# Kernel optimization log

Measured on AMD Instinct MI355X. Metric: run time of the kernel, lower is better.

## Reference

```python
import jax, jax.numpy as jnp
import numpy as np


def setup_inputs() -> dict:
    key = jax.random.key(0)
    ks = jax.random.split(key, 8)
    C, R = 256, 16
    Cqk = C // R  # 16
    B, H, W = 8, 64, 64
    x = jax.random.normal(ks[0], (B, C, H, W), dtype=jnp.float32)
    # 1x1 conv weights stored as [out, in] (kernel dims squeezed)
    s = 1.0 / np.sqrt(C)
    Wq = jax.random.uniform(ks[1], (Cqk, C), minval=-s, maxval=s, dtype=jnp.float32)
    bq = jax.random.uniform(ks[2], (Cqk,), minval=-s, maxval=s, dtype=jnp.float32)
    Wk = jax.random.uniform(ks[3], (Cqk, C), minval=-s, maxval=s, dtype=jnp.float32)
    bk = jax.random.uniform(ks[4], (Cqk,), minval=-s, maxval=s, dtype=jnp.float32)
    Wv = jax.random.uniform(ks[5], (C, C), minval=-s, maxval=s, dtype=jnp.float32)
    bv = jax.random.uniform(ks[6], (C,), minval=-s, maxval=s, dtype=jnp.float32)
    gamma = jnp.float32(0.1)  # nonzero so the attention branch affects output
    return {"x": x, "Wq": Wq, "bq": bq, "Wk": Wk, "bk": bk, "Wv": Wv, "bv": bv, "gamma": gamma}


def reference(x, Wq, bq, Wk, bk, Wv, bv, gamma):
    B, C, H, W = x.shape
    N = H * W
    xf = x.reshape(B, C, N)  # [B, C, N]
    # 1x1 convs == per-pixel linear over channel dim
    q = jnp.einsum('oc,bcn->bon', Wq, xf) + bq[None, :, None]  # [B, Cqk, N]
    k = jnp.einsum('oc,bcn->bon', Wk, xf) + bk[None, :, None]  # [B, Cqk, N]
    v = jnp.einsum('oc,bcn->bon', Wv, xf) + bv[None, :, None]  # [B, C, N]
    # scores[b, i, j] = q[:, i] . k[:, j]; no scale factor (faithful to source)
    scores = jnp.einsum('bdn,bdm->bnm', q, k)  # [B, N, N]
    attn = jax.nn.softmax(scores, axis=-1)
    # y[b, c, i] = sum_j v[b, c, j] * attn[b, i, j]
    y = jnp.einsum('bcm,bnm->bcn', v, attn).reshape(B, C, H, W)
    return x + gamma * y
```

## Files before the change

### kernel.cpp

```cpp
#include <hip/hip_runtime.h>
#include <hip/hip_bf16.h>
#include <math.h>

typedef short bf16x8 __attribute__((ext_vector_type(8)));
typedef float f32x4 __attribute__((ext_vector_type(4)));

#define MFMA_B16(A, B, C) __builtin_amdgcn_mfma_f32_16x16x32_bf16(A, B, C, 0, 0, 0)

#define NBATCH 8
#define CIN 256
#define NPIX 4096

__device__ __forceinline__ unsigned short f2b(float f) {
    union { float f; unsigned int u; } v;
    v.f = f;
    return (unsigned short)((v.u + 0x7fffu + ((v.u >> 16) & 1u)) >> 16);
}

__global__ __launch_bounds__(256, 2) void qkv_kernel(
    const float* __restrict__ x,
    const float* __restrict__ Wq, const float* __restrict__ bq,
    const float* __restrict__ Wk, const float* __restrict__ bk,
    const float* __restrict__ Wv, const float* __restrict__ bv,
    unsigned short* __restrict__ qT, unsigned short* __restrict__ kT,
    unsigned short* __restrict__ vv)
{
    constexpr int XSTR = 264;
    __shared__ __align__(16) unsigned short xs[64 * XSTR];
    const int b     = blockIdx.x >> 6;
    const int nbase = (blockIdx.x & 63) * 64;
    const int tid = threadIdx.x;
    const int w  = tid >> 6;
    const int l  = tid & 63;
    const int g  = l >> 4;
    const int ln = l & 15;

    {
        const float* xp = x + (size_t)b * CIN * NPIX + nbase + l;
        unsigned short* xsp = xs + l * XSTR + w * 64;
        #pragma unroll
        for (int cc = 0; cc < 32; ++cc) {
            float v0 = xp[(size_t)(w * 64 + 2 * cc)     * NPIX];
            float v1 = xp[(size_t)(w * 64 + 2 * cc + 1) * NPIX];
            unsigned int pk = (unsigned int)f2b(v0) | ((unsigned int)f2b(v1) << 16);
            *(unsigned int*)(xsp + 2 * cc) = pk;
        }
    }
    __syncthreads();

    const f32x4 vzero = {0.f, 0.f, 0.f, 0.f};
    f32x4 acc[4][4];
    f32x4 accq[4];
    #pragma unroll
    for (int i = 0; i < 4; ++i) {
        accq[i] = vzero;
        #pragma unroll
        for (int j = 0; j < 4; ++j) acc[i][j] = vzero;
    }

    for (int ks = 0; ks < 8; ++ks) {
        const int k0 = ks * 32;
        bf16x8 xf[4];
        #pragma unroll
        for (int nt = 0; nt < 4; ++nt)
            xf[nt] = *(const bf16x8*)(xs + (nt * 16 + ln) * XSTR + k0 + g * 8);
        #pragma unroll
        for (int ct = 0; ct < 4; ++ct) {
            const float* wp = Wv + (size_t)(w * 64 + ct * 16 + ln) * CIN + k0 + g * 8;
            bf16x8 wf;
            #pragma unroll
            for (int j = 0; j < 8; ++j) wf[j] = (short)f2b(wp[j]);
            #pragma unroll
            for (int nt = 0; nt < 4; ++nt)
                acc[ct][nt] = MFMA_B16(wf, xf[nt], acc[ct][nt]);
        }
        if (w < 2) {
            const float* wqk = (w == 0 ? Wq : Wk) + (size_t)ln * CIN + k0 + g * 8;
            bf16x8 wf;
            #pragma unroll
            for (int j = 0; j < 8; ++j) wf[j] = (short)f2b(wqk[j]);
            #pragma unroll
            for (int nt = 0; nt < 4; ++nt)
                accq[nt] = MFMA_B16(wf, xf[nt], accq[nt]);
        }
    }

    #pragma unroll
    for (int ct = 0; ct < 4; ++ct) {
        #pragma unroll
        for (int r = 0; r < 4; ++r) {
            const int c = w * 64 + ct * 16 + g * 4 + r;
            const float bias = bv[c];
            #pragma unroll
            for (int nt = 0; nt < 4; ++nt)
                vv[((size_t)b * CIN + c) * NPIX + nbase + nt * 16 + ln] =
                    f2b(acc[ct][nt][r] + bias);
        }
    }
    if (w < 2) {
        unsigned short* oq = (w == 0 ? qT : kT);
        const float* bias  = (w == 0 ? bq : bk);
        #pragma unroll
        for (int r = 0; r < 4; ++r) {
            const int d = g * 4 + r;
            const float bi = bias[d];
            #pragma unroll
            for (int nt = 0; nt < 4; ++nt)
                oq[((size_t)b * NPIX + nbase + nt * 16 + ln) * 32 + d] =
                    f2b(accq[nt][r] + bi);
        }
    } else {
        unsigned short* oq = (w == 2 ? qT : kT);
        unsigned short* p  = oq + ((size_t)b * NPIX + nbase + l) * 32 + 16;
        uint4 z; z.x = 0; z.y = 0; z.z = 0; z.w = 0;
        *(uint4*)p       = z;
        *(uint4*)(p + 8) = z;
    }
}

__global__ __launch_bounds__(256, 2) void attn_kernel(
    const float* __restrict__ x, const float* __restrict__ gamma_p,
    const unsigned short* __restrict__ qT, const unsigned short* __restrict__ kT,
    const unsigned short* __restrict__ vv, float* __restrict__ out)
{
    constexpr int PSTR = 72;
    __shared__ __align__(16) unsigned short P_lds[64 * PSTR];
    __shared__ __align__(16) float smax[64 * 4];
    __shared__ __align__(16) float ssum[64 * 4];
    const int b     = blockIdx.x & 7;
    const int qbase = (blockIdx.x >> 3) * 64;
    const int tid = threadIdx.x;
    const int w  = tid >> 6;
    const int l  = tid & 63;
    const int g  = l >> 4;
    const int ln = l & 15;
    const float gamma = *gamma_p;

    bf16x8 qf[4];
    #pragma unroll
    for (int qt = 0; qt < 4; ++qt)
        qf[qt] = *(const bf16x8*)(qT + ((size_t)b * NPIX + qbase + qt * 16 + ln) * 32 + g * 8);

    const f32x4 vzero = {0.f, 0.f, 0.f, 0.f};
    f32x4 acc[4][4];
    #pragma unroll
    for (int i = 0; i < 4; ++i) {
        #pragma unroll
        for (int j = 0; j < 4; ++j) acc[i][j] = vzero;
    }
    float m_run[4] = {-INFINITY, -INFINITY, -INFINITY, -INFINITY};
    float l_run[4] = {0.f, 0.f, 0.f, 0.f};

    for (int kt = 0; kt < 64; ++kt) {
        const int k0 = kt * 64;
        const bf16x8 kf = *(const bf16x8*)(kT + ((size_t)b * NPIX + k0 + w * 16 + ln) * 32 + g * 8);
        f32x4 s[4];
        #pragma unroll
        for (int qt = 0; qt < 4; ++qt)
            s[qt] = MFMA_B16(kf, qf[qt], vzero);

        float pm[4];
        #pragma unroll
        for (int qt = 0; qt < 4; ++qt) {
            float m = fmaxf(fmaxf(s[qt][0], s[qt][1]), fmaxf(s[qt][2], s[qt][3]));
            m = fmaxf(m, __shfl_xor(m, 16));
            m = fmaxf(m, __shfl_xor(m, 32));
            pm[qt] = m;
        }
        if (g == 0) {
            #pragma unroll
            for (int qt = 0; qt < 4; ++qt) smax[(qt * 16 + ln) * 4 + w] = pm[qt];
        }
        __syncthreads();

        float m_new[4], scale[4], ps[4];
        #pragma unroll
        for (int qt = 0; qt < 4; ++qt) {
            f32x4 t = *(const f32x4*)(smax + (qt * 16 + ln) * 4);
            float tm = fmaxf(fmaxf(t[0], t[1]), fmaxf(t[2], t[3]));
            m_new[qt] = fmaxf(m_run[qt], tm);
            scale[qt] = __expf(m_run[qt] - m_new[qt]);
        }
        #pragma unroll
        for (int qt = 0; qt < 4; ++qt) {
            float p0 = __expf(s[qt][0] - m_new[qt]);
            float p1 = __expf(s[qt][1] - m_new[qt]);
            float p2 = __expf(s[qt][2] - m_new[qt]);
            float p3 = __expf(s[qt][3] - m_new[qt]);
            float sum = (p0 + p1) + (p2 + p3);
            sum += __shfl_xor(sum, 16);
            sum += __shfl_xor(sum, 32);
            ps[qt] = sum;
            uint2 pk;
            pk.x = (unsigned int)f2b(p0) | ((unsigned int)f2b(p1) << 16);
            pk.y = (unsigned int)f2b(p2) | ((unsigned int)f2b(p3) << 16);
            *(uint2*)(P_lds + (qt * 16 + ln) * PSTR + w * 16 + g * 4) = pk;
        }
        if (g == 0) {
            #pragma unroll
            for (int qt = 0; qt < 4; ++qt) ssum[(qt * 16 + ln) * 4 + w] = ps[qt];
        }
        __syncthreads();

        #pragma unroll
        for (int qt = 0; qt < 4; ++qt) {
            f32x4 t = *(const f32x4*)(ssum + (qt * 16 + ln) * 4);
            l_run[qt] = l_run[qt] * scale[qt] + ((t[0] + t[1]) + (t[2] + t[3]));
            m_run[qt] = m_new[qt];
            #pragma unroll
            for (int ct = 0; ct < 4; ++ct) {
                acc[qt][ct][0] *= scale[qt];
                acc[qt][ct][1] *= scale[qt];
                acc[qt][ct][2] *= scale[qt];
                acc[qt][ct][3] *= scale[qt];
            }
        }

        #pragma unroll
        for (int kk = 0; kk < 2; ++kk) {
            bf16x8 pf[4];
            #pragma unroll
            for (int qt = 0; qt < 4; ++qt)
                pf[qt] = *(const bf16x8*)(P_lds + (qt * 16 + ln) * PSTR + kk * 32 + g * 8);
            #pragma unroll
            for (int ct = 0; ct < 4; ++ct) {
                const bf16x8 vf = *(const bf16x8*)(
                    vv + ((size_t)b * CIN + w * 64 + ct * 16 + ln) * NPIX + k0 + kk * 32 + g * 8);
                #pragma unroll
                for (int qt = 0; qt < 4; ++qt)
                    acc[qt][ct] = MFMA_B16(vf, pf[qt], acc[qt][ct]);
            }
        }
    }

    #pragma unroll
    for (int qt = 0; qt < 4; ++qt) {
        const float inv = 1.0f / l_run[qt];
        const int n = qbase + qt * 16 + ln;
        #pragma unroll
        for (int ct = 0; ct < 4; ++ct) {
            #pragma unroll
            for (int r = 0; r < 4; ++r) {
                const int c = w * 64 + ct * 16 + g * 4 + r;
                const size_t idx = ((size_t)b * CIN + c) * NPIX + n;
                out[idx] = x[idx] + gamma * (acc[qt][ct][r] * inv);
            }
        }
    }
}

extern "C" void kernel_launch(void* const* d_in, const int* in_sizes, int n_in,
                              void* d_out, int out_size, void* d_ws, size_t ws_size,
                              hipStream_t stream) {
    const float* x     = (const float*)d_in[0];
    const float* Wq    = (const float*)d_in[1];
    const float* bq    = (const float*)d_in[2];
    const float* Wk    = (const float*)d_in[3];
    const float* bk    = (const float*)d_in[4];
    const float* Wv    = (const float*)d_in[5];
    const float* bv    = (const float*)d_in[6];
    const float* gamma = (const float*)d_in[7];

    unsigned short* qT = (unsigned short*)d_ws;
    unsigned short* kT = qT + (size_t)NBATCH * NPIX * 32;
    unsigned short* vv = kT + (size_t)NBATCH * NPIX * 32;

    qkv_kernel<<<512, 256, 0, stream>>>(x, Wq, bq, Wk, bk, Wv, bv, qT, kT, vv);
    attn_kernel<<<512, 256, 0, stream>>>(x, gamma, qT, kT, vv, (float*)d_out);
}
```

Before: 331.7 us.

## Restructure attention to barrier-free per-wave softmax with lazy rescaling and prepacked weights

The attention kernel is reorganized so each wave owns 32 query rows across all 64 keys, with a 2x2 split over query and channel halves. This removes the shared-memory max/sum exchange and both block barriers; P is rearranged into the MFMA operand layout with cross-lane shuffles instead of going through LDS. Softmax switches to exp2 with log2(e) folded into Wq and bq, uses a hardware bf16 pack instruction, and only rescales the accumulators when the running max grows by more than a threshold. A new pre-kernel converts the weights to bf16 once so qkv_kernel loads packed weights instead of converting them per tile. The trade-offs are an extra launch, duplicated K loads and QK MFMAs across the waves that share a query half, and more shuffle traffic.

```diff
diff --git a/kernel.cpp b/kernel.cpp
--- a/kernel.cpp
+++ b/kernel.cpp
@@ -10,6 +10,8 @@
 #define NBATCH 8
 #define CIN 256
 #define NPIX 4096
+#define L2E 1.4426950408889634f
+#define THR2 8.0f
 
 __device__ __forceinline__ unsigned short f2b(float f) {
     union { float f; unsigned int u; } v;
@@ -17,11 +19,31 @@
     return (unsigned short)((v.u + 0x7fffu + ((v.u >> 16) & 1u)) >> 16);
 }
 
+__device__ __forceinline__ unsigned int cvtpk(float lo, float hi) {
+    unsigned int r;
+    asm volatile("v_cvt_pk_bf16_f32 %0, %1, %2" : "=v"(r) : "v"(lo), "v"(hi));
+    return r;
+}
+
+__global__ void packw_kernel(const float* __restrict__ Wq, const float* __restrict__ Wk,
+                             const float* __restrict__ Wv,
+                             unsigned short* __restrict__ wv_bf,
+                             unsigned short* __restrict__ wqk_bf) {
+    int t = blockIdx.x * 256 + threadIdx.x;
+    if (t < 65536) {
+        wv_bf[t] = f2b(Wv[t]);
+    } else {
+        int u = t - 65536;
+        int r = u >> 8, c = u & 255;
+        float v = (r < 16) ? Wq[r * 256 + c] * L2E : Wk[(r - 16) * 256 + c];
+        wqk_bf[u] = f2b(v);
+    }
+}
+
 __global__ __launch_bounds__(256, 2) void qkv_kernel(
     const float* __restrict__ x,
-    const float* __restrict__ Wq, const float* __restrict__ bq,
-    const float* __restrict__ Wk, const float* __restrict__ bk,
-    const float* __restrict__ Wv, const float* __restrict__ bv,
+    const unsigned short* __restrict__ wv_bf, const unsigned short* __restrict__ wqk_bf,
+    const float* __restrict__ bq, const float* __restrict__ bk, const float* __restrict__ bv,
     unsigned short* __restrict__ qT, unsigned short* __restrict__ kT,
     unsigned short* __restrict__ vv)
 {
@@ -66,22 +88,16 @@
             xf[nt] = *(const bf16x8*)(xs + (nt * 16 + ln) * XSTR + k0 + g * 8);
         #pragma unroll
         for (int ct = 0; ct < 4; ++ct) {
-            const float* wp = Wv + (size_t)(w * 64 + ct * 16 + ln) * CIN + k0 + g * 8;
-            bf16x8 wf;
-            #pragma unroll
-            for (int j = 0; j < 8; ++j) wf[j] = (short)f2b(wp[j]);
+            const bf16x8 wf = *(const bf16x8*)(wv_bf + (size_t)(w * 64 + ct * 16 + ln) * CIN + k0 + g * 8);
             #pragma unroll
             for (int nt = 0; nt < 4; ++nt)
                 acc[ct][nt] = MFMA_B16(wf, xf[nt], acc[ct][nt]);
         }
         if (w < 2) {
-            const float* wqk = (w == 0 ? Wq : Wk) + (size_t)ln * CIN + k0 + g * 8;
-            bf16x8 wf;
-            #pragma unroll
-            for (int j = 0; j < 8; ++j) wf[j] = (short)f2b(wqk[j]);
-            #pragma unroll
-            for (int nt = 0; nt < 4; ++nt)
-                accq[nt] = MFMA_B16(wf, xf[nt], accq[nt]);
+            const bf16x8 wfq = *(const bf16x8*)(wqk_bf + (size_t)(w * 16 + ln) * CIN + k0 + g * 8);
+            #pragma unroll
+            for (int nt = 0; nt < 4; ++nt)
+                accq[nt] = MFMA_B16(wfq, xf[nt], accq[nt]);
         }
     }
 
@@ -99,11 +115,10 @@
     }
     if (w < 2) {
         unsigned short* oq = (w == 0 ? qT : kT);
-        const float* bias  = (w == 0 ? bq : bk);
         #pragma unroll
         for (int r = 0; r < 4; ++r) {
             const int d = g * 4 + r;
-            const float bi = bias[d];
+            const float bi = (w == 0 ? bq[d] * L2E : bk[d]);
             #pragma unroll
             for (int nt = 0; nt < 4; ++nt)
                 oq[((size_t)b * NPIX + nbase + nt * 16 + ln) * 32 + d] =
@@ -123,125 +138,131 @@
     const unsigned short* __restrict__ qT, const unsigned short* __restrict__ kT,
     const unsigned short* __restrict__ vv, float* __restrict__ out)
 {
-    constexpr int PSTR = 72;
-    __shared__ __align__(16) unsigned short P_lds[64 * PSTR];
-    __shared__ __align__(16) float smax[64 * 4];
-    __shared__ __align__(16) float ssum[64 * 4];
     const int b     = blockIdx.x & 7;
     const int qbase = (blockIdx.x >> 3) * 64;
     const int tid = threadIdx.x;
-    const int w  = tid >> 6;
-    const int l  = tid & 63;
-    const int g  = l >> 4;
-    const int ln = l & 15;
+    const int wid = tid >> 6;
+    const int wq  = wid & 1;
+    const int wc  = wid >> 1;
+    const int l   = tid & 63;
+    const int ln  = l & 15;
+    const int g   = l >> 4;
     const float gamma = *gamma_p;
 
-    bf16x8 qf[4];
-    #pragma unroll
-    for (int qt = 0; qt < 4; ++qt)
-        qf[qt] = *(const bf16x8*)(qT + ((size_t)b * NPIX + qbase + qt * 16 + ln) * 32 + g * 8);
+    const int srcA = ln + ((g & 1) << 5);
+    const int srcB = srcA + 16;
+    const bool hi  = (g >> 1) != 0;
+
+    bf16x8 qf[2];
+    #pragma unroll
+    for (int qt = 0; qt < 2; ++qt)
+        qf[qt] = *(const bf16x8*)(qT + ((size_t)b * NPIX + qbase + wq * 32 + qt * 16 + ln) * 32 + g * 8);
 
     const f32x4 vzero = {0.f, 0.f, 0.f, 0.f};
-    f32x4 acc[4][4];
-    #pragma unroll
-    for (int i = 0; i < 4; ++i) {
-        #pragma unroll
-        for (int j = 0; j < 4; ++j) acc[i][j] = vzero;
-    }
-    float m_run[4] = {-INFINITY, -INFINITY, -INFINITY, -INFINITY};
-    float l_run[4] = {0.f, 0.f, 0.f, 0.f};
+    f32x4 acc[2][8];
+    #pragma unroll
+    for (int i = 0; i < 2; ++i)
+        #pragma unroll
+        for (int j = 0; j < 8; ++j) acc[i][j] = vzero;
+    float m_run[2]  = {-INFINITY, -INFINITY};
+    float l_part[2] = {0.f, 0.f};
+
+    const unsigned short* kbase = kT + (size_t)b * NPIX * 32;
+    const unsigned short* vbase = vv + ((size_t)b * CIN + wc * 128) * NPIX;
 
     for (int kt = 0; kt < 64; ++kt) {
         const int k0 = kt * 64;
-        const bf16x8 kf = *(const bf16x8*)(kT + ((size_t)b * NPIX + k0 + w * 16 + ln) * 32 + g * 8);
-        f32x4 s[4];
-        #pragma unroll
-        for (int qt = 0; qt < 4; ++qt)
-            s[qt] = MFMA_B16(kf, qf[qt], vzero);
-
-        float pm[4];
-        #pragma unroll
-        for (int qt = 0; qt < 4; ++qt) {
-            float m = fmaxf(fmaxf(s[qt][0], s[qt][1]), fmaxf(s[qt][2], s[qt][3]));
-            m = fmaxf(m, __shfl_xor(m, 16));
-            m = fmaxf(m, __shfl_xor(m, 32));
-            pm[qt] = m;
-        }
-        if (g == 0) {
-            #pragma unroll
-            for (int qt = 0; qt < 4; ++qt) smax[(qt * 16 + ln) * 4 + w] = pm[qt];
-        }
-        __syncthreads();
-
-        float m_new[4], scale[4], ps[4];
-        #pragma unroll
-        for (int qt = 0; qt < 4; ++qt) {
-            f32x4 t = *(const f32x4*)(smax + (qt * 16 + ln) * 4);
-            float tm = fmaxf(fmaxf(t[0], t[1]), fmaxf(t[2], t[3]));
-            m_new[qt] = fmaxf(m_run[qt], tm);
-            scale[qt] = __expf(m_run[qt] - m_new[qt]);
-        }
-        #pragma unroll
-        for (int qt = 0; qt < 4; ++qt) {
-            float p0 = __expf(s[qt][0] - m_new[qt]);
-            float p1 = __expf(s[qt][1] - m_new[qt]);
-            float p2 = __expf(s[qt][2] - m_new[qt]);
-            float p3 = __expf(s[qt][3] - m_new[qt]);
-            float sum = (p0 + p1) + (p2 + p3);
-            sum += __shfl_xor(sum, 16);
-            sum += __shfl_xor(sum, 32);
-            ps[qt] = sum;
-            uint2 pk;
-            pk.x = (unsigned int)f2b(p0) | ((unsigned int)f2b(p1) << 16);
-            pk.y = (unsigned int)f2b(p2) | ((unsigned int)f2b(p3) << 16);
-            *(uint2*)(P_lds + (qt * 16 + ln) * PSTR + w * 16 + g * 4) = pk;
-        }
-        if (g == 0) {
-            #pragma unroll
-            for (int qt = 0; qt < 4; ++qt) ssum[(qt * 16 + ln) * 4 + w] = ps[qt];
-        }
-        __syncthreads();
-
-        #pragma unroll
-        for (int qt = 0; qt < 4; ++qt) {
-            f32x4 t = *(const f32x4*)(ssum + (qt * 16 + ln) * 4);
-            l_run[qt] = l_run[qt] * scale[qt] + ((t[0] + t[1]) + (t[2] + t[3]));
-            m_run[qt] = m_new[qt];
-            #pragma unroll
-            for (int ct = 0; ct < 4; ++ct) {
-                acc[qt][ct][0] *= scale[qt];
-                acc[qt][ct][1] *= scale[qt];
-                acc[qt][ct][2] *= scale[qt];
-                acc[qt][ct][3] *= scale[qt];
+        bf16x8 kf[4];
+        #pragma unroll
+        for (int ws = 0; ws < 4; ++ws)
+            kf[ws] = *(const bf16x8*)(kbase + (size_t)(k0 + 16 * ws + ln) * 32 + g * 8);
+
+        f32x4 s[2][4];
+        #pragma unroll
+        for (int qt = 0; qt < 2; ++qt)
+            #pragma unroll
+            for (int ws = 0; ws < 4; ++ws)
+                s[qt][ws] = MFMA_B16(kf[ws], qf[qt], vzero);
+
+        unsigned int pk[2][4][2];
+        #pragma unroll
+        for (int qt = 0; qt < 2; ++qt) {
+            float pml = fmaxf(fmaxf(s[qt][0][0], s[qt][0][1]), fmaxf(s[qt][0][2], s[qt][0][3]));
+            #pragma unroll
+            for (int ws = 1; ws < 4; ++ws)
+                pml = fmaxf(pml, fmaxf(fmaxf(s[qt][ws][0], s[qt][ws][1]),
+                                       fmaxf(s[qt][ws][2], s[qt][ws][3])));
+            if (__any(pml > m_run[qt] + THR2)) {
+                float pm = fmaxf(pml, __shfl_xor(pml, 16));
+                pm = fmaxf(pm, __shfl_xor(pm, 32));
+                float mn = fmaxf(m_run[qt], pm);
+                float sc = exp2f(m_run[qt] - mn);
+                #pragma unroll
+                for (int ct = 0; ct < 8; ++ct) acc[qt][ct] *= sc;
+                l_part[qt] *= sc;
+                m_run[qt] = mn;
+            }
+            float ts = 0.f;
+            #pragma unroll
+            for (int ws = 0; ws < 4; ++ws)
+                #pragma unroll
+                for (int r = 0; r < 4; ++r) {
+                    float p = exp2f(s[qt][ws][r] - m_run[qt]);
+                    s[qt][ws][r] = p;
+                    ts += p;
+                }
+            l_part[qt] += ts;
+            #pragma unroll
+            for (int ws = 0; ws < 4; ++ws) {
+                pk[qt][ws][0] = cvtpk(s[qt][ws][0], s[qt][ws][1]);
+                pk[qt][ws][1] = cvtpk(s[qt][ws][2], s[qt][ws][3]);
             }
         }
 
         #pragma unroll
         for (int kk = 0; kk < 2; ++kk) {
-            bf16x8 pf[4];
-            #pragma unroll
-            for (int qt = 0; qt < 4; ++qt)
-                pf[qt] = *(const bf16x8*)(P_lds + (qt * 16 + ln) * PSTR + kk * 32 + g * 8);
-            #pragma unroll
-            for (int ct = 0; ct < 4; ++ct) {
+            bf16x8 pf[2];
+            #pragma unroll
+            for (int qt = 0; qt < 2; ++qt) {
+                unsigned int aL0 = __shfl((int)pk[qt][2 * kk][0],     srcA);
+                unsigned int aL1 = __shfl((int)pk[qt][2 * kk][1],     srcA);
+                unsigned int aH0 = __shfl((int)pk[qt][2 * kk + 1][0], srcA);
+                unsigned int aH1 = __shfl((int)pk[qt][2 * kk + 1][1], srcA);
+                unsigned int bL0 = __shfl((int)pk[qt][2 * kk][0],     srcB);
+                unsigned int bL1 = __shfl((int)pk[qt][2 * kk][1],     srcB);
+                unsigned int bH0 = __shfl((int)pk[qt][2 * kk + 1][0], srcB);
+                unsigned int bH1 = __shfl((int)pk[qt][2 * kk + 1][1], srcB);
+                union { unsigned int u[4]; bf16x8 v; } pu;
+                pu.u[0] = hi ? aH0 : aL0;
+                pu.u[1] = hi ? aH1 : aL1;
+                pu.u[2] = hi ? bH0 : bL0;
+                pu.u[3] = hi ? bH1 : bL1;
+                pf[qt] = pu.v;
+            }
+            __builtin_amdgcn_s_setprio(1);
+            #pragma unroll
+            for (int ct = 0; ct < 8; ++ct) {
                 const bf16x8 vf = *(const bf16x8*)(
-                    vv + ((size_t)b * CIN + w * 64 + ct * 16 + ln) * NPIX + k0 + kk * 32 + g * 8);
-                #pragma unroll
-                for (int qt = 0; qt < 4; ++qt)
-                    acc[qt][ct] = MFMA_B16(vf, pf[qt], acc[qt][ct]);
-            }
-        }
-    }
-
-    #pragma unroll
-    for (int qt = 0; qt < 4; ++qt) {
-        const float inv = 1.0f / l_run[qt];
-        const int n = qbase + qt * 16 + ln;
-        #pragma unroll
-        for (int ct = 0; ct < 4; ++ct) {
+                    vbase + (size_t)(ct * 16 + ln) * NPIX + k0 + kk * 32 + g * 8);
+                acc[0][ct] = MFMA_B16(vf, pf[0], acc[0][ct]);
+                acc[1][ct] = MFMA_B16(vf, pf[1], acc[1][ct]);
+            }
+            __builtin_amdgcn_s_setprio(0);
+        }
+    }
+
+    #pragma unroll
+    for (int qt = 0; qt < 2; ++qt) {
+        float lt = l_part[qt];
+        lt += __shfl_xor(lt, 16);
+        lt += __shfl_xor(lt, 32);
+        const float inv = 1.0f / lt;
+        const int n = qbase + wq * 32 + qt * 16 + ln;
+        #pragma unroll
+        for (int ct = 0; ct < 8; ++ct) {
             #pragma unroll
             for (int r = 0; r < 4; ++r) {
-                const int c = w * 64 + ct * 16 + g * 4 + r;
+                const int c = wc * 128 + ct * 16 + g * 4 + r;
                 const size_t idx = ((size_t)b * CIN + c) * NPIX + n;
                 out[idx] = x[idx] + gamma * (acc[qt][ct][r] * inv);
             }
@@ -261,10 +282,13 @@
     const float* bv    = (const float*)d_in[6];
     const float* gamma = (const float*)d_in[7];
 
-    unsigned short* qT = (unsigned short*)d_ws;
-    unsigned short* kT = qT + (size_t)NBATCH * NPIX * 32;
-    unsigned short* vv = kT + (size_t)NBATCH * NPIX * 32;
-
-    qkv_kernel<<<512, 256, 0, stream>>>(x, Wq, bq, Wk, bk, Wv, bv, qT, kT, vv);
-    attn_kernel<<<512, 256, 0, stream>>>(x, gamma, qT, kT, vv, (float*)d_out);
-}
+    unsigned short* qTp  = (unsigned short*)d_ws;
+    unsigned short* kTp  = qTp + (size_t)NBATCH * NPIX * 32;
+    unsigned short* vvp  = kTp + (size_t)NBATCH * NPIX * 32;
+    unsigned short* wvb  = vvp + (size_t)NBATCH * CIN * NPIX;
+    unsigned short* wqkb = wvb + 256 * 256;
+
+    packw_kernel<<<288, 256, 0, stream>>>(Wq, Wk, Wv, wvb, wqkb);
+    qkv_kernel<<<512, 256, 0, stream>>>(x, wvb, wqkb, bq, bk, bv, qTp, kTp, vvp);
+    attn_kernel<<<512, 256, 0, stream>>>(x, gamma, qTp, kTp, vvp, (float*)d_out);
+}
```

After: 371.9 us. 12.1% more time.
